# Performance work log

Measured on AMD Instinct MI355X. Metric: run time of the kernel, lower is better.

The kernel has to match this reference:

```python
import jax, jax.numpy as jnp
import numpy as np

B, N, P, K, C = 8, 4096, 4096, 32, 128  # batch, points, npoint, neighbors, channels (=mlp[-1])
W_OUT = 16  # weightnet output channels (from Linear(16*mlp[-1], mlp[-1]))
EPS = 1e-5


def setup_inputs() -> dict:
    key = jax.random.key(0)
    ks = jax.random.split(key, 9)
    xyz = jax.random.normal(ks[0], (B, P, 3), jnp.float32)
    points = jax.random.normal(ks[1], (B, N, C), jnp.float32)
    local_coordinates = jax.random.normal(ks[2], (B, P, K, 3), jnp.float32)
    neighbor_lists = jax.random.randint(ks[3], (B, P, K), 0, N)
    data_idx = jax.random.randint(ks[4], (B,), 0, B)
    Ww = jax.random.normal(ks[5], (3, W_OUT), jnp.float32) * 0.1   # weightnet (pointwise linear 3->16)
    bw = jnp.zeros((W_OUT,), jnp.float32)
    Wl = jax.random.normal(ks[6], (W_OUT * C, C), jnp.float32) * 0.02  # nn.Linear(16*mlp[-1], mlp[-1])
    bl = jnp.zeros((C,), jnp.float32)
    gamma = jnp.ones((C,), jnp.float32)   # BatchNorm1d weight
    beta = jnp.zeros((C,), jnp.float32)   # BatchNorm1d bias
    return {"xyz": xyz, "points": points, "local_coordinates": local_coordinates,
            "neighbor_lists": neighbor_lists, "data_idx": data_idx,
            "Ww": Ww, "bw": bw, "Wl": Wl, "bl": bl, "gamma": gamma, "beta": beta}


def reference(xyz, points, local_coordinates, neighbor_lists, data_idx, Ww, bw, Wl, bl, gamma, beta):
    b, p, k, _ = local_coordinates.shape
    c = points.shape[-1]
    # weightnet: pointwise map of 3-D local coordinates to 16 weight channels -> [B,P,K,16]
    weights = local_coordinates @ Ww + bw
    # irregular neighbor gather: data[b,p,k,:] = points[b, neighbor_lists[b,p,k], :] -> [B,P,K,C]
    data = points[jnp.arange(b)[:, None, None], neighbor_lists]
    # per-point weighted aggregation over K neighbors: [B,P,C,16] -> flatten to [B,P,C*16]
    new_points = jnp.einsum('bpkc,bpkw->bpcw', data, weights).reshape(b, p, c * weights.shape[-1])
    # batch reindex via data_idx
    new_points = new_points[data_idx]
    # linear tail: [B,P,C]
    new_points = new_points @ Wl + bl
    # BatchNorm1d over channel dim (training-mode batch stats), then ReLU: [B,C,P]
    x = new_points.transpose(0, 2, 1)
    mean = x.mean(axis=(0, 2), keepdims=True)
    var = x.var(axis=(0, 2), keepdims=True)
    x = (x - mean) * jax.lax.rsqrt(var + EPS) * gamma[None, :, None] + beta[None, :, None]
    return xyz, jax.nn.relu(x)
```

## Files before the change

kernel.cpp:

```cpp
#include <hip/hip_runtime.h>

#define Bn 8
#define Nn 4096
#define Pn 4096
#define Kn 32
#define Cn 128

using float4v = __attribute__((ext_vector_type(4))) float;
using short8  = __attribute__((ext_vector_type(8))) short;

__device__ __forceinline__ unsigned short bf16b(float f) {
  union { float f; unsigned u; } v; v.f = f;
  unsigned r = v.u + 0x7FFFu + ((v.u >> 16) & 1u);
  return (unsigned short)(r >> 16);
}

__device__ __forceinline__ unsigned pkhi(float x, float y) {
  return __builtin_amdgcn_perm(__float_as_uint(y), __float_as_uint(x), 0x07060302u);
}

__global__ __launch_bounds__(256) void prep(const float* __restrict__ Wl,
                                            unsigned short* __restrict__ WlT,
                                            const float* __restrict__ xyz,
                                            float* __restrict__ out,
                                            float* __restrict__ gacc) {
  __shared__ unsigned short tile[128 * 33];
  const int t = threadIdx.x, blk = blockIdx.x;
  if (blk < 64) {
#pragma unroll
    for (int i = 0; i < 16; ++i) {
      int idx = i * 256 + t;
      int kl = idx >> 7, n = idx & 127;
      tile[n * 33 + kl] = bf16b(Wl[(size_t)(blk * 32 + kl) * 128 + n]);
    }
    __syncthreads();
#pragma unroll
    for (int i = 0; i < 16; ++i) {
      int idx = i * 256 + t;
      int n = idx >> 5, kl = idx & 31;
      WlT[(size_t)n * 2048 + blk * 32 + kl] = tile[n * 33 + kl];
    }
  } else {
    if (blk == 64) gacc[t] = 0.f;
    const int i0 = (blk - 64) * 3072 + t * 12;
#pragma unroll
    for (int i = 0; i < 3; ++i)
      *(float4v*)(out + i0 + i * 4) = *(const float4v*)(xyz + i0 + i * 4);
  }
}

__global__ __launch_bounds__(256, 4) void fused(
    const float* __restrict__ points, const float* __restrict__ lc,
    const int* __restrict__ nl, const int* __restrict__ didx,
    const float* __restrict__ Ww, const float* __restrict__ bwv,
    const unsigned short* __restrict__ WlT, const float* __restrict__ blv,
    float* __restrict__ xout, float* __restrict__ gacc) {
  __shared__ unsigned short Mlds[32 * 256 + 7424];
  __shared__ int nlds[32 * 32];
  __shared__ float red[256];

  const int t = threadIdx.x, lane = t & 63, w = t >> 6;
  const int l15 = lane & 15, q = lane >> 4;
  const int b = blockIdx.x & 7;
  const int pg = blockIdx.x >> 3;
  const int p0 = pg * 32;
  const int db = didx[b];
  const char* __restrict__ pbase = (const char*)(points + (size_t)db * Nn * Cn);

  if (blockIdx.x == 0xFFFFFFFFu) ((volatile unsigned short*)Mlds)[32 * 256 + t] = 0;

  {
    int4 nv = *(const int4*)(nl + (size_t)(db * Pn + p0) * Kn + t * 4);
    nv.x <<= 9; nv.y <<= 9; nv.z <<= 9; nv.w <<= 9;
    *(int4*)&nlds[t * 4] = nv;
  }

  const float Ww0 = Ww[l15], Ww1 = Ww[16 + l15], Ww2 = Ww[32 + l15];
  const float bw0 = bwv[l15];

  short8 af[8];
#pragma unroll
  for (int i = 0; i < 8; ++i) {
    const int p = p0 + w * 8 + i;
    const int pk = (db * Pn + p) * Kn;
    const float* __restrict__ lcp = lc + (size_t)(pk + q * 8) * 3;
    float la[24];
#pragma unroll
    for (int v = 0; v < 6; ++v) *(float4v*)&la[v * 4] = *(const float4v*)(lcp + v * 4);
#pragma unroll
    for (int j = 0; j < 8; ++j) {
      float ww = bw0 + la[3 * j] * Ww0 + la[3 * j + 1] * Ww1 + la[3 * j + 2] * Ww2;
      af[i][j] = (short)bf16b(ww);
    }
  }

  float4v acc[2][2];
#pragma unroll
  for (int pt = 0; pt < 2; ++pt)
#pragma unroll
    for (int nt = 0; nt < 2; ++nt) acc[pt][nt] = (float4v){0.f, 0.f, 0.f, 0.f};

  __syncthreads();

  const unsigned short* __restrict__ bpt =
      WlT + (size_t)(w * 32 + l15) * 2048 + q * 8;
  const unsigned cvoff = (unsigned)(l15 * 4);

#define ISSUE(i, ct, fdst)                                                 \
  {                                                                        \
    const int pi_ = w * 8 + (i);                                           \
    int nk_[8];                                                            \
    *(int4*)&nk_[0] = *(const int4*)&nlds[pi_ * 32 + q * 8];               \
    *(int4*)&nk_[4] = *(const int4*)&nlds[pi_ * 32 + q * 8 + 4];           \
    _Pragma("unroll") for (int j = 0; j < 8; ++j)                          \
        fdst[j] = *(const float*)(pbase + ((unsigned)nk_[j] + cvoff +      \
                                           (unsigned)((ct) * 64)));        \
  }

#define FIN(i, fsrc)                                                       \
  {                                                                        \
    const int pi_ = w * 8 + (i);                                           \
    union { short8 s; unsigned u[4]; } bv_;                                \
    bv_.u[0] = pkhi(fsrc[0], fsrc[1]);                                     \
    bv_.u[1] = pkhi(fsrc[2], fsrc[3]);                                     \
    bv_.u[2] = pkhi(fsrc[4], fsrc[5]);                                     \
    bv_.u[3] = pkhi(fsrc[6], fsrc[7]);                                     \
    float4v d_ = {0.f, 0.f, 0.f, 0.f};                                     \
    d_ = __builtin_amdgcn_mfma_f32_16x16x32_bf16(af[i], bv_.s, d_, 0, 0, 0); \
    const unsigned off_ = (unsigned)(pi_ * 512 + ((l15 * 32 + q * 8) ^     \
        ((((pi_ & 7) ^ (l15 & 7)) & 7) << 4)));                            \
    uint2 u_;                                                              \
    u_.x = pkhi(d_[0], d_[1]);                                             \
    u_.y = pkhi(d_[2], d_[3]);                                             \
    *(uint2*)((char*)Mlds + off_) = u_;                                    \
  }

  float fb[4][8];

  for (int ct = 0; ct < 8; ++ct) {
    ISSUE(0, ct, fb[0])
    ISSUE(1, ct, fb[1])
    ISSUE(2, ct, fb[2])
    ISSUE(3, ct, fb[3])
#pragma unroll
    for (int i = 0; i < 8; ++i) {
      FIN(i, fb[i & 3])
      if (i + 4 < 8) ISSUE(i + 4, ct, fb[i & 3])
    }
    __syncthreads();
    const unsigned short* __restrict__ bp = bpt + ct * 256;
    __builtin_amdgcn_s_setprio(1);
#pragma unroll
    for (int ks = 0; ks < 8; ++ks) {
      const unsigned ax = (unsigned)((ks * 64 + q * 16) ^
          ((((l15 & 7) ^ ((ks * 2 + (q >> 1)) & 7)) & 7) << 4));
      short8 a0 = *(const short8*)((const char*)Mlds + l15 * 512 + ax);
      short8 a1 = *(const short8*)((const char*)Mlds + (16 + l15) * 512 + ax);
      short8 b0 = *(const short8*)(bp + ks * 32);
      short8 b1 = *(const short8*)(bp + 32768 + ks * 32);
      acc[0][0] = __builtin_amdgcn_mfma_f32_16x16x32_bf16(a0, b0, acc[0][0], 0, 0, 0);
      acc[0][1] = __builtin_amdgcn_mfma_f32_16x16x32_bf16(a0, b1, acc[0][1], 0, 0, 0);
      acc[1][0] = __builtin_amdgcn_mfma_f32_16x16x32_bf16(a1, b0, acc[1][0], 0, 0, 0);
      acc[1][1] = __builtin_amdgcn_mfma_f32_16x16x32_bf16(a1, b1, acc[1][1], 0, 0, 0);
    }
    __builtin_amdgcn_s_setprio(0);
    __syncthreads();
  }
#undef ISSUE
#undef FIN

#pragma unroll
  for (int nt = 0; nt < 2; ++nt) {
    const int ch = w * 32 + nt * 16 + l15;
    const float bb = blv[ch];
    float s = 0.f, sq = 0.f;
#pragma unroll
    for (int pt = 0; pt < 2; ++pt) {
      float4v o;
#pragma unroll
      for (int r = 0; r < 4; ++r) {
        float v = acc[pt][nt][r] + bb; o[r] = v; s += v; sq += v * v;
      }
      *(float4v*)(xout + ((size_t)(b * Cn + ch)) * Pn + p0 + pt * 16 + q * 4) = o;
    }
    s += __shfl_xor(s, 16); s += __shfl_xor(s, 32);
    sq += __shfl_xor(sq, 16); sq += __shfl_xor(sq, 32);
    if (lane < 16) { red[ch] = s; red[128 + ch] = sq; }
  }
  __syncthreads();
  atomicAdd(&gacc[t], red[t]);
}

__global__ __launch_bounds__(256) void finalize_ln(float* __restrict__ x,
                                                   const float* __restrict__ gacc,
                                                   const float* __restrict__ gamma,
                                                   const float* __restrict__ beta) {
  const int idx = blockIdx.x * 256 + threadIdx.x;
  const int fi = idx * 4;
  const int c = (fi >> 12) & 127;
  const float inv = 1.f / 32768.f;
  const float mean = gacc[c] * inv;
  const float var = gacc[128 + c] * inv - mean * mean;
  const float scale = rsqrtf(var + 1e-5f) * gamma[c];
  const float shift = beta[c] - mean * scale;
  float4v v = *(float4v*)(x + fi);
#pragma unroll
  for (int r = 0; r < 4; ++r) v[r] = fmaxf(v[r] * scale + shift, 0.f);
  *(float4v*)(x + fi) = v;
}

extern "C" void kernel_launch(void* const* d_in, const int* in_sizes, int n_in,
                              void* d_out, int out_size, void* d_ws, size_t ws_size,
                              hipStream_t stream) {
  const float* xyz    = (const float*)d_in[0];
  const float* points = (const float*)d_in[1];
  const float* lc     = (const float*)d_in[2];
  const int*   nl     = (const int*)d_in[3];
  const int*   didx   = (const int*)d_in[4];
  const float* Ww     = (const float*)d_in[5];
  const float* bw     = (const float*)d_in[6];
  const float* Wl     = (const float*)d_in[7];
  const float* bl     = (const float*)d_in[8];
  const float* gamma  = (const float*)d_in[9];
  const float* beta   = (const float*)d_in[10];

  float* out  = (float*)d_out;
  float* xout = out + (size_t)Bn * Pn * 3;
  unsigned short* WlT = (unsigned short*)d_ws;
  float* gacc = (float*)((char*)d_ws + (size_t)512 * 1024);

  prep<<<96, 256, 0, stream>>>(Wl, WlT, xyz, out, gacc);
  fused<<<1024, 256, 0, stream>>>(points, lc, nl, didx, Ww, bw, WlT, bl,
                                  xout, gacc);
  finalize_ln<<<4096, 256, 0, stream>>>(xout, gacc, gamma, beta);
}
```

Before: 191.6 us.

## Split fused kernel into producer and consumer warps with double-buffered LDS

Blocks grow to 512 threads. Four producer waves gather neighbor features and run the weightnet MFMA into one of two LDS buffers. Four consumer waves run the Wl GEMM on the other buffer one step behind, with register prefetch of the WlT fragments. The goal is to overlap the irregular gather with the tensor-core GEMM instead of serialising them inside each wave, at the cost of more registers and LDS per block, which may lower occupancy.

```diff
diff --git a/kernel.cpp b/kernel.cpp
--- a/kernel.cpp
+++ b/kernel.cpp
@@ -49,13 +49,13 @@
   }
 }
 
-__global__ __launch_bounds__(256, 4) void fused(
+__global__ __launch_bounds__(512, 4) void fused(
     const float* __restrict__ points, const float* __restrict__ lc,
     const int* __restrict__ nl, const int* __restrict__ didx,
     const float* __restrict__ Ww, const float* __restrict__ bwv,
     const unsigned short* __restrict__ WlT, const float* __restrict__ blv,
     float* __restrict__ xout, float* __restrict__ gacc) {
-  __shared__ unsigned short Mlds[32 * 256 + 7424];
+  __shared__ unsigned short Mlds[2][32 * 256];
   __shared__ int nlds[32 * 32];
   __shared__ float red[256];
 
@@ -66,31 +66,31 @@
   const int p0 = pg * 32;
   const int db = didx[b];
   const char* __restrict__ pbase = (const char*)(points + (size_t)db * Nn * Cn);
-
-  if (blockIdx.x == 0xFFFFFFFFu) ((volatile unsigned short*)Mlds)[32 * 256 + t] = 0;
+  const bool prod = (w < 4);
 
   {
-    int4 nv = *(const int4*)(nl + (size_t)(db * Pn + p0) * Kn + t * 4);
-    nv.x <<= 9; nv.y <<= 9; nv.z <<= 9; nv.w <<= 9;
-    *(int4*)&nlds[t * 4] = nv;
-  }
-
-  const float Ww0 = Ww[l15], Ww1 = Ww[16 + l15], Ww2 = Ww[32 + l15];
-  const float bw0 = bwv[l15];
+    int2 nv = *(const int2*)(nl + (size_t)(db * Pn + p0) * Kn + t * 2);
+    nv.x <<= 9; nv.y <<= 9;
+    *(int2*)&nlds[t * 2] = nv;
+  }
 
   short8 af[8];
-#pragma unroll
-  for (int i = 0; i < 8; ++i) {
-    const int p = p0 + w * 8 + i;
-    const int pk = (db * Pn + p) * Kn;
-    const float* __restrict__ lcp = lc + (size_t)(pk + q * 8) * 3;
-    float la[24];
-#pragma unroll
-    for (int v = 0; v < 6; ++v) *(float4v*)&la[v * 4] = *(const float4v*)(lcp + v * 4);
-#pragma unroll
-    for (int j = 0; j < 8; ++j) {
-      float ww = bw0 + la[3 * j] * Ww0 + la[3 * j + 1] * Ww1 + la[3 * j + 2] * Ww2;
-      af[i][j] = (short)bf16b(ww);
+  if (prod) {
+    const float Ww0 = Ww[l15], Ww1 = Ww[16 + l15], Ww2 = Ww[32 + l15];
+    const float bw0 = bwv[l15];
+#pragma unroll
+    for (int i = 0; i < 8; ++i) {
+      const int p = p0 + w * 8 + i;
+      const int pk = (db * Pn + p) * Kn;
+      const float* __restrict__ lcp = lc + (size_t)(pk + q * 8) * 3;
+      float la[24];
+#pragma unroll
+      for (int v = 0; v < 6; ++v) *(float4v*)&la[v * 4] = *(const float4v*)(lcp + v * 4);
+#pragma unroll
+      for (int j = 0; j < 8; ++j) {
+        float ww = bw0 + la[3 * j] * Ww0 + la[3 * j + 1] * Ww1 + la[3 * j + 2] * Ww2;
+        af[i][j] = (short)bf16b(ww);
+      }
     }
   }
 
@@ -103,7 +103,7 @@
   __syncthreads();
 
   const unsigned short* __restrict__ bpt =
-      WlT + (size_t)(w * 32 + l15) * 2048 + q * 8;
+      WlT + (size_t)((w & 3) * 32 + l15) * 2048 + q * 8;
   const unsigned cvoff = (unsigned)(l15 * 4);
 
 #define ISSUE(i, ct, fdst)                                                 \
@@ -117,7 +117,7 @@
                                            (unsigned)((ct) * 64)));        \
   }
 
-#define FIN(i, fsrc)                                                       \
+#define FIN(i, bsel, fsrc)                                                 \
   {                                                                        \
     const int pi_ = w * 8 + (i);                                           \
     union { short8 s; unsigned u[4]; } bv_;                                \
@@ -127,8 +127,8 @@
     bv_.u[3] = pkhi(fsrc[6], fsrc[7]);                                     \
     float4v d_ = {0.f, 0.f, 0.f, 0.f};                                     \
     d_ = __builtin_amdgcn_mfma_f32_16x16x32_bf16(af[i], bv_.s, d_, 0, 0, 0); \
-    const unsigned off_ = (unsigned)(pi_ * 512 + ((l15 * 32 + q * 8) ^     \
-        ((((pi_ & 7) ^ (l15 & 7)) & 7) << 4)));                            \
+    const unsigned off_ = (unsigned)((bsel) * 16384 + pi_ * 512 +          \
+        ((l15 * 32 + q * 8) ^ ((((pi_ & 7) ^ (l15 & 7)) & 7) << 4)));      \
     uint2 u_;                                                              \
     u_.x = pkhi(d_[0], d_[1]);                                             \
     u_.y = pkhi(d_[2], d_[3]);                                             \
@@ -137,58 +137,76 @@
 
   float fb[4][8];
 
-  for (int ct = 0; ct < 8; ++ct) {
-    ISSUE(0, ct, fb[0])
-    ISSUE(1, ct, fb[1])
-    ISSUE(2, ct, fb[2])
-    ISSUE(3, ct, fb[3])
-#pragma unroll
-    for (int i = 0; i < 8; ++i) {
-      FIN(i, fb[i & 3])
-      if (i + 4 < 8) ISSUE(i + 4, ct, fb[i & 3])
-    }
-    __syncthreads();
-    const unsigned short* __restrict__ bp = bpt + ct * 256;
-    __builtin_amdgcn_s_setprio(1);
-#pragma unroll
-    for (int ks = 0; ks < 8; ++ks) {
-      const unsigned ax = (unsigned)((ks * 64 + q * 16) ^
-          ((((l15 & 7) ^ ((ks * 2 + (q >> 1)) & 7)) & 7) << 4));
-      short8 a0 = *(const short8*)((const char*)Mlds + l15 * 512 + ax);
-      short8 a1 = *(const short8*)((const char*)Mlds + (16 + l15) * 512 + ax);
-      short8 b0 = *(const short8*)(bp + ks * 32);
-      short8 b1 = *(const short8*)(bp + 32768 + ks * 32);
-      acc[0][0] = __builtin_amdgcn_mfma_f32_16x16x32_bf16(a0, b0, acc[0][0], 0, 0, 0);
-      acc[0][1] = __builtin_amdgcn_mfma_f32_16x16x32_bf16(a0, b1, acc[0][1], 0, 0, 0);
-      acc[1][0] = __builtin_amdgcn_mfma_f32_16x16x32_bf16(a1, b0, acc[1][0], 0, 0, 0);
-      acc[1][1] = __builtin_amdgcn_mfma_f32_16x16x32_bf16(a1, b1, acc[1][1], 0, 0, 0);
-    }
-    __builtin_amdgcn_s_setprio(0);
+#pragma unroll 1
+  for (int it = 0; it < 9; ++it) {
+    if (prod) {
+      if (it < 8) {
+        const int ct = it, bsel = it & 1;
+        ISSUE(0, ct, fb[0])
+        ISSUE(1, ct, fb[1])
+        ISSUE(2, ct, fb[2])
+        ISSUE(3, ct, fb[3])
+#pragma unroll
+        for (int i = 0; i < 8; ++i) {
+          FIN(i, bsel, fb[i & 3])
+          if (i + 4 < 8) ISSUE(i + 4, ct, fb[i & 3])
+        }
+      }
+    } else {
+      if (it > 0) {
+        const int ct = it - 1;
+        const char* mb = (const char*)Mlds + (ct & 1) * 16384;
+        const unsigned short* __restrict__ bp = bpt + ct * 256;
+        short8 b0A = *(const short8*)(bp);
+        short8 b1A = *(const short8*)(bp + 32768);
+        __builtin_amdgcn_s_setprio(1);
+#pragma unroll
+        for (int ks = 0; ks < 8; ++ks) {
+          short8 b0B, b1B;
+          if (ks < 7) {
+            b0B = *(const short8*)(bp + (ks + 1) * 32);
+            b1B = *(const short8*)(bp + 32768 + (ks + 1) * 32);
+          }
+          const unsigned ax = (unsigned)((ks * 64 + q * 16) ^
+              ((((l15 & 7) ^ ((ks * 2 + (q >> 1)) & 7)) & 7) << 4));
+          short8 a0 = *(const short8*)(mb + l15 * 512 + ax);
+          short8 a1 = *(const short8*)(mb + (16 + l15) * 512 + ax);
+          acc[0][0] = __builtin_amdgcn_mfma_f32_16x16x32_bf16(a0, b0A, acc[0][0], 0, 0, 0);
+          acc[0][1] = __builtin_amdgcn_mfma_f32_16x16x32_bf16(a0, b1A, acc[0][1], 0, 0, 0);
+          acc[1][0] = __builtin_amdgcn_mfma_f32_16x16x32_bf16(a1, b0A, acc[1][0], 0, 0, 0);
+          acc[1][1] = __builtin_amdgcn_mfma_f32_16x16x32_bf16(a1, b1A, acc[1][1], 0, 0, 0);
+          b0A = b0B; b1A = b1B;
+        }
+        __builtin_amdgcn_s_setprio(0);
+      }
+    }
     __syncthreads();
   }
 #undef ISSUE
 #undef FIN
 
-#pragma unroll
-  for (int nt = 0; nt < 2; ++nt) {
-    const int ch = w * 32 + nt * 16 + l15;
-    const float bb = blv[ch];
-    float s = 0.f, sq = 0.f;
-#pragma unroll
-    for (int pt = 0; pt < 2; ++pt) {
-      float4v o;
-#pragma unroll
-      for (int r = 0; r < 4; ++r) {
-        float v = acc[pt][nt][r] + bb; o[r] = v; s += v; sq += v * v;
-      }
-      *(float4v*)(xout + ((size_t)(b * Cn + ch)) * Pn + p0 + pt * 16 + q * 4) = o;
-    }
-    s += __shfl_xor(s, 16); s += __shfl_xor(s, 32);
-    sq += __shfl_xor(sq, 16); sq += __shfl_xor(sq, 32);
-    if (lane < 16) { red[ch] = s; red[128 + ch] = sq; }
+  if (!prod) {
+#pragma unroll
+    for (int nt = 0; nt < 2; ++nt) {
+      const int ch = (w & 3) * 32 + nt * 16 + l15;
+      const float bb = blv[ch];
+      float s = 0.f, sq = 0.f;
+#pragma unroll
+      for (int pt = 0; pt < 2; ++pt) {
+        float4v o;
+#pragma unroll
+        for (int r = 0; r < 4; ++r) {
+          float v = acc[pt][nt][r] + bb; o[r] = v; s += v; sq += v * v;
+        }
+        *(float4v*)(xout + ((size_t)(b * Cn + ch)) * Pn + p0 + pt * 16 + q * 4) = o;
+      }
+      s += __shfl_xor(s, 16); s += __shfl_xor(s, 32);
+      sq += __shfl_xor(sq, 16); sq += __shfl_xor(sq, 32);
+      if (lane < 16) { red[ch] = s; red[128 + ch] = sq; }
+    }
   }
   __syncthreads();
-  atomicAdd(&gacc[t], red[t]);
+  if (t < 256) atomicAdd(&gacc[t], red[t]);
 }
 
 __global__ __launch_bounds__(256) void finalize_ln(float* __restrict__ x,
@@ -230,7 +248,7 @@
   float* gacc = (float*)((char*)d_ws + (size_t)512 * 1024);
 
   prep<<<96, 256, 0, stream>>>(Wl, WlT, xyz, out, gacc);
-  fused<<<1024, 256, 0, stream>>>(points, lc, nl, didx, Ww, bw, WlT, bl,
+  fused<<<1024, 512, 0, stream>>>(points, lc, nl, didx, Ww, bw, WlT, bl,
                                   xout, gacc);
   finalize_ln<<<4096, 256, 0, stream>>>(xout, gacc, gamma, beta);
 }
```

New measurement: 193.6 us. No clear change (+1.0%).
